# Optimization experiments

Hardware: AMD Instinct MI355X
Metric: run time of the kernel (lower is better)

The kernel has to match this reference:

```python
import jax, jax.numpy as jnp
import numpy as np
from jax import lax

UNITS = 64
LAYERS = 4

def _lstm_layer(x, Wx, U, b):
    # x: [B,T,F]; Keras gate order i,f,c,o; activation=relu, recurrent_activation=sigmoid
    B = x.shape[0]
    xz = jnp.einsum('btf,fg->btg', x, Wx) + b  # precompute input projections [B,T,4U]
    def step(carry, xz_t):
        h, c = carry
        z = xz_t + h @ U
        i, f, g, o = jnp.split(z, 4, axis=-1)
        c = jax.nn.sigmoid(f) * c + jax.nn.sigmoid(i) * jax.nn.relu(g)
        h = jax.nn.sigmoid(o) * jax.nn.relu(c)
        return (h, c), h
    h0 = jnp.zeros((B, UNITS), dtype=x.dtype)
    c0 = jnp.zeros((B, UNITS), dtype=x.dtype)
    _, hs = lax.scan(step, (h0, c0), jnp.swapaxes(xz, 0, 1))
    return jnp.swapaxes(hs, 0, 1)  # [B,T,U]

def setup_inputs() -> dict:
    key = jax.random.key(0)
    ks = jax.random.split(key, 1 + 3 * LAYERS + 2)
    B, T, F = 1024, 512, 1
    d = {'x': jax.random.normal(ks[0], (B, T, F), dtype=jnp.float32)}
    fin = F
    for l in range(LAYERS):
        d[f'Wx{l}'] = jax.random.normal(ks[1 + 3 * l], (fin, 4 * UNITS), dtype=jnp.float32) * 0.05
        d[f'U{l}'] = jax.random.normal(ks[2 + 3 * l], (UNITS, 4 * UNITS), dtype=jnp.float32) * 0.05
        d[f'b{l}'] = jnp.zeros((4 * UNITS,), dtype=jnp.float32)
        fin = UNITS
    d['Wd'] = jax.random.normal(ks[-2], (UNITS, 1), dtype=jnp.float32) * 0.05
    d['bd'] = jnp.zeros((1,), dtype=jnp.float32)
    return d

def reference(x, Wx0, U0, b0, Wx1, U1, b1, Wx2, U2, b2, Wx3, U3, b3, Wd, bd):
    # Dropout is identity at inference.
    h = x
    for Wx, U, b in ((Wx0, U0, b0), (Wx1, U1, b1), (Wx2, U2, b2), (Wx3, U3, b3)):
        h = _lstm_layer(h, Wx, U, b)
    h_last = h[:, -1, :]  # return_sequences=False on last LSTM
    return h_last @ Wd + bd  # [B,1]
```

## Files before the change

kernel.cpp:

```cpp
#include <hip/hip_runtime.h>
#include <stdint.h>

#define TT 512

typedef __fp16   f16x8  __attribute__((ext_vector_type(8)));
typedef float    f32x4  __attribute__((ext_vector_type(4)));
typedef __fp16   fp16x2 __attribute__((ext_vector_type(2)));
typedef uint32_t u32x2  __attribute__((ext_vector_type(2)));

__device__ __forceinline__ f32x4 mfma16(f16x8 a, f16x8 b, f32x4 c) {
    return __builtin_amdgcn_mfma_f32_16x16x32_f16(a, b, c, 0, 0, 0);
}
__device__ __forceinline__ uint32_t pkf16(float a, float b) {
    fp16x2 h = __builtin_amdgcn_cvt_pkrtz(a, b);
    return __builtin_bit_cast(uint32_t, h);
}

#define REP8(M) M(0)M(1)M(2)M(3)M(4)M(5)M(6)M(7)

#define GA(SRC, T, F, SC) (f16x8){ \
  (__fp16)((SRC)[(32*(F)+8*quad+0)*256 + 16*(T)+l15] * (SC)), \
  (__fp16)((SRC)[(32*(F)+8*quad+1)*256 + 16*(T)+l15] * (SC)), \
  (__fp16)((SRC)[(32*(F)+8*quad+2)*256 + 16*(T)+l15] * (SC)), \
  (__fp16)((SRC)[(32*(F)+8*quad+3)*256 + 16*(T)+l15] * (SC)), \
  (__fp16)((SRC)[(32*(F)+8*quad+4)*256 + 16*(T)+l15] * (SC)), \
  (__fp16)((SRC)[(32*(F)+8*quad+5)*256 + 16*(T)+l15] * (SC)), \
  (__fp16)((SRC)[(32*(F)+8*quad+6)*256 + 16*(T)+l15] * (SC)), \
  (__fp16)((SRC)[(32*(F)+8*quad+7)*256 + 16*(T)+l15] * (SC)) }

#define DECLT(j) f16x8 uA##j##_0, uA##j##_1, wA##j##_0, wA##j##_1; f32x4 bias##j;
#define LOADT(j) { \
  const int Tg_ = ((j)>>1)*4 + 2*h + ((j)&1); \
  const float sc_ = (((j)>>1) == 2) ? 1.0f : -1.4426950408889634f; \
  uA##j##_0 = GA(Uw, Tg_, 0, sc_); uA##j##_1 = GA(Uw, Tg_, 1, sc_); \
  bias##j = (f32x4){ bw_[16*Tg_ + 4*quad + 0] * sc_, bw_[16*Tg_ + 4*quad + 1] * sc_, \
                     bw_[16*Tg_ + 4*quad + 2] * sc_, bw_[16*Tg_ + 4*quad + 3] * sc_ }; \
  if (l > 0) { wA##j##_0 = GA(Wsrc, Tg_, 0, sc_); wA##j##_1 = GA(Wsrc, Tg_, 1, sc_); } \
  else { wA##j##_0 = __builtin_bit_cast(f16x8, (f32x4){ \
           Wx0[16*Tg_+4*quad+0] * sc_, Wx0[16*Tg_+4*quad+1] * sc_, \
           Wx0[16*Tg_+4*quad+2] * sc_, Wx0[16*Tg_+4*quad+3] * sc_ }); \
         wA##j##_1 = wA##j##_0; } }

#define MW0(j) acc##j = mfma16(wA##j##_0, xBp0, bias##j);
#define MW1(j) acc##j = mfma16(wA##j##_1, xBp1, acc##j);
#define MX(j)  acc##j = bias##j + __builtin_bit_cast(f32x4, wA##j##_0) * xvp4;
#define MU0(j) acc##j = mfma16(uA##j##_0, hB0, acc##j);
#define MU1(j) acc##j = mfma16(uA##j##_1, hB1, acc##j);

#define MFMA_SEG(t_) { \
  const __fp16* hp_ = hb_l + (((t_)-1)&7)*1152 + l15*72 + 8*quad; \
  f16x8 hB0 = *(const f16x8*)hp_; \
  f16x8 hB1 = *(const f16x8*)(hp_ + 32); \
  if (l > 0) { REP8(MW0) REP8(MW1) } \
  else       { f32x4 xvp4 = {xvp, xvp, xvp, xvp}; REP8(MX) } \
  REP8(MU0) \
  REP8(MU1) }

#define GATES(qp, Ai, Af, Ag, Ao, CST, SAVEK, HK) { \
  f32x4 ei_, ef_, eo_; \
  _Pragma("unroll") for (int r_ = 0; r_ < 4; ++r_) { \
    ei_[r_] = __builtin_amdgcn_exp2f(Ai[r_]); \
    ef_[r_] = __builtin_amdgcn_exp2f(Af[r_]); \
    eo_[r_] = __builtin_amdgcn_exp2f(Ao[r_]); \
  } \
  f32x4 si_, sf_, so_; \
  _Pragma("unroll") for (int r_ = 0; r_ < 4; ++r_) { \
    si_[r_] = __builtin_amdgcn_rcpf(1.0f + ei_[r_]); \
    sf_[r_] = __builtin_amdgcn_rcpf(1.0f + ef_[r_]); \
    so_[r_] = __builtin_amdgcn_rcpf(1.0f + eo_[r_]); \
  } \
  const f32x4 z4_ = {0.f, 0.f, 0.f, 0.f}; \
  f32x4 rg_ = __builtin_elementwise_max(Ag, z4_); \
  f32x4 cv_ = sf_ * CST + si_ * rg_; \
  CST = cv_; \
  f32x4 hv_ = so_ * __builtin_elementwise_max(cv_, z4_); \
  u32x2 pv_ = { pkf16(hv_[0], hv_[1]), pkf16(hv_[2], hv_[3]) }; \
  *(u32x2*)(hw_ + 16*(qp)) = pv_; \
  if (SAVEK) HK = hv_; }

#define GATE_SEG(tg_, SV_) { \
  __fp16* hw_ = hb_l + ((tg_)&7)*1152 + l15*72 + 32*h + 4*quad; \
  GATES(0, acc0, acc2, acc4, acc6, cst0, SV_, hK0) \
  GATES(1, acc1, acc3, acc5, acc7, cst1, SV_, hK1) }

#define WAITGE(cache, idx, need) \
  while ((cache) < (need)) \
    (cache) = __hip_atomic_load(&Pf[idx], __ATOMIC_ACQUIRE, __HIP_MEMORY_SCOPE_WORKGROUP);

__global__ __launch_bounds__(512)
__attribute__((amdgpu_waves_per_eu(2, 2)))
void lstm_phase(
    const float* __restrict__ x,
    const float* __restrict__ Wx0, const float* __restrict__ U0, const float* __restrict__ b0,
    const float* __restrict__ Wx1, const float* __restrict__ U1, const float* __restrict__ b1,
    const float* __restrict__ Wx2, const float* __restrict__ U2, const float* __restrict__ b2,
    const float* __restrict__ Wx3, const float* __restrict__ U3, const float* __restrict__ b3,
    const float* __restrict__ Wd,  const float* __restrict__ bd,
    float* __restrict__ out)
{
    extern __shared__ uint32_t smem[];
    __fp16* hb16 = (__fp16*)smem;
    float*  xs   = (float*)(smem + 18432);
    float*  red  = (float*)(smem + 27136);
    int*    Pf   = (int*)(smem + 27168);

    const int tid  = threadIdx.x;
    const int lane = tid & 63;
    const int l15  = lane & 15;
    const int quad = lane >> 4;
    const int wv   = tid >> 6;
    const int l    = wv >> 1;
    const int h    = wv & 1;
    const int b0i  = blockIdx.x * 16;

    for (int i = tid; i < 27176; i += 512) smem[i] = 0;
    __syncthreads();
    for (int i = tid; i < 16 * TT; i += 512) {
        int row = i >> 9, t_ = i & (TT - 1);
        xs[t_ * 17 + row] = x[(b0i + row) * TT + t_];
    }

    const float* Uw   = (l == 0) ? U0 : (l == 1) ? U1 : (l == 2) ? U2 : U3;
    const float* bw_  = (l == 0) ? b0 : (l == 1) ? b1 : (l == 2) ? b2 : b3;
    const float* Wsrc = (l == 1) ? Wx1 : (l == 2) ? Wx2 : (l == 3) ? Wx3 : U0;

    REP8(DECLT)
    REP8(LOADT)

    f32x4 acc0, acc1, acc2, acc3, acc4, acc5, acc6, acc7;
    f32x4 cst0 = {0,0,0,0}, cst1 = {0,0,0,0};
    f32x4 hK0  = {0,0,0,0}, hK1  = {0,0,0,0};

    __fp16* hb_l  = hb16 + l * 9216;
    const __fp16* hb_in = hb16 + (l > 0 ? (l - 1) * 9216 : 0);

    f16x8 xBp0 = {}, xBp1 = {};
    float xvp = 0.f;

    __syncthreads();

    if (l == 0) xvp = xs[l15];

    int pA0 = 0, pA1 = 0, pP = 0, pC0 = 0, pC1 = 0;

    for (int t = 0; t < TT; ++t) {
        if (l > 0) {
            WAITGE(pA0, 2*l - 2, t + 1)
            WAITGE(pA1, 2*l - 1, t + 1)
            const __fp16* xp_ = hb_in + (t & 7) * 1152 + l15 * 72 + 8 * quad;
            xBp0 = *(const f16x8*)xp_;
            xBp1 = *(const f16x8*)(xp_ + 32);
        }
        if (t > 0) WAITGE(pP, 2*l + 1 - h, t)
        if (l < 3 && t >= 8) {
            WAITGE(pC0, 2*l + 2, t - 7)
            WAITGE(pC1, 2*l + 3, t - 7)
        }
        __builtin_amdgcn_s_setprio(1);
        MFMA_SEG(t)
        __builtin_amdgcn_s_setprio(0);
        {
            const bool sv_ = (l == 3) && (t == TT - 1);
            GATE_SEG(t, sv_)
        }
        __hip_atomic_store(&Pf[2*l + h], t + 1, __ATOMIC_RELEASE, __HIP_MEMORY_SCOPE_WORKGROUP);
        if (l == 0 && t + 1 < TT) xvp = xs[(t + 1) * 17 + l15];
    }

    __syncthreads();

    if (l == 3) {
        float p = 0.f;
        #pragma unroll
        for (int r = 0; r < 4; ++r) {
            p += hK0[r] * Wd[32 * h + 4 * quad + r];
            p += hK1[r] * Wd[32 * h + 16 + 4 * quad + r];
        }
        p += __shfl_down(p, 32, 64);
        p += __shfl_down(p, 16, 64);
        if (lane < 16) red[h * 16 + lane] = p;
    }
    __syncthreads();
    if (wv == 6 && lane < 16) out[b0i + lane] = red[lane] + red[16 + lane] + bd[0];
}

extern "C" void kernel_launch(void* const* d_in, const int* in_sizes, int n_in,
                              void* d_out, int out_size, void* d_ws, size_t ws_size,
                              hipStream_t stream) {
    const float* x   = (const float*)d_in[0];
    const float* Wx0 = (const float*)d_in[1];
    const float* U0  = (const float*)d_in[2];
    const float* b0  = (const float*)d_in[3];
    const float* Wx1 = (const float*)d_in[4];
    const float* U1  = (const float*)d_in[5];
    const float* b1  = (const float*)d_in[6];
    const float* Wx2 = (const float*)d_in[7];
    const float* U2  = (const float*)d_in[8];
    const float* b2  = (const float*)d_in[9];
    const float* Wx3 = (const float*)d_in[10];
    const float* U3  = (const float*)d_in[11];
    const float* b3  = (const float*)d_in[12];
    const float* Wd  = (const float*)d_in[13];
    const float* bd  = (const float*)d_in[14];
    float* out = (float*)d_out;

    static const int kLds = 27176 * 4;
    (void)hipFuncSetAttribute((const void*)lstm_phase,
                              hipFuncAttributeMaxDynamicSharedMemorySize, kLds);
    hipLaunchKernelGGL(lstm_phase, dim3(64), dim3(512), kLds, stream,
                       x, Wx0, U0, b0, Wx1, U1, b1, Wx2, U2, b2, Wx3, U3, b3,
                       Wd, bd, out);
}
```

Baseline: 638.5 us.

## Split each LSTM layer across four waves instead of two per workgroup

Doubles the block to 1024 threads so each layer's gate computation is spread over four waves, each owning a 16-unit slice, with half as many MFMAs and gate evaluations per wave per timestep. Biases move from registers to LDS and are reloaded every step to free registers for the higher wave count. Per-wave progress flags replace per-pair flags, so each wave now polls three sibling flags plus four upstream and four downstream flags. The aim is to shorten the serial per-step critical path, at the cost of more synchronisation polling and LDS traffic.

New measurement: 1.095 ms. +71.4%, slower.

```diff
diff --git a/kernel.cpp b/kernel.cpp
--- a/kernel.cpp
+++ b/kernel.cpp
@@ -16,7 +16,7 @@
     return __builtin_bit_cast(uint32_t, h);
 }
 
-#define REP8(M) M(0)M(1)M(2)M(3)M(4)M(5)M(6)M(7)
+#define REP4(M) M(0)M(1)M(2)M(3)
 
 #define GA(SRC, T, F, SC) (f16x8){ \
   (__fp16)((SRC)[(32*(F)+8*quad+0)*256 + 16*(T)+l15] * (SC)), \
@@ -28,13 +28,11 @@
   (__fp16)((SRC)[(32*(F)+8*quad+6)*256 + 16*(T)+l15] * (SC)), \
   (__fp16)((SRC)[(32*(F)+8*quad+7)*256 + 16*(T)+l15] * (SC)) }
 
-#define DECLT(j) f16x8 uA##j##_0, uA##j##_1, wA##j##_0, wA##j##_1; f32x4 bias##j;
+#define DECLT(j) f16x8 uA##j##_0, uA##j##_1, wA##j##_0, wA##j##_1;
 #define LOADT(j) { \
-  const int Tg_ = ((j)>>1)*4 + 2*h + ((j)&1); \
-  const float sc_ = (((j)>>1) == 2) ? 1.0f : -1.4426950408889634f; \
+  const int Tg_ = 4*(j) + w; \
+  const float sc_ = ((j) == 2) ? 1.0f : -1.4426950408889634f; \
   uA##j##_0 = GA(Uw, Tg_, 0, sc_); uA##j##_1 = GA(Uw, Tg_, 1, sc_); \
-  bias##j = (f32x4){ bw_[16*Tg_ + 4*quad + 0] * sc_, bw_[16*Tg_ + 4*quad + 1] * sc_, \
-                     bw_[16*Tg_ + 4*quad + 2] * sc_, bw_[16*Tg_ + 4*quad + 3] * sc_ }; \
   if (l > 0) { wA##j##_0 = GA(Wsrc, Tg_, 0, sc_); wA##j##_1 = GA(Wsrc, Tg_, 1, sc_); } \
   else { wA##j##_0 = __builtin_bit_cast(f16x8, (f32x4){ \
            Wx0[16*Tg_+4*quad+0] * sc_, Wx0[16*Tg_+4*quad+1] * sc_, \
@@ -48,20 +46,24 @@
 #define MU1(j) acc##j = mfma16(uA##j##_1, hB1, acc##j);
 
 #define MFMA_SEG(t_) { \
+  f32x4 bias0 = *(const f32x4*)(bsl +   0); \
+  f32x4 bias1 = *(const f32x4*)(bsl +  64); \
+  f32x4 bias2 = *(const f32x4*)(bsl + 128); \
+  f32x4 bias3 = *(const f32x4*)(bsl + 192); \
   const __fp16* hp_ = hb_l + (((t_)-1)&7)*1152 + l15*72 + 8*quad; \
   f16x8 hB0 = *(const f16x8*)hp_; \
   f16x8 hB1 = *(const f16x8*)(hp_ + 32); \
-  if (l > 0) { REP8(MW0) REP8(MW1) } \
-  else       { f32x4 xvp4 = {xvp, xvp, xvp, xvp}; REP8(MX) } \
-  REP8(MU0) \
-  REP8(MU1) }
-
-#define GATES(qp, Ai, Af, Ag, Ao, CST, SAVEK, HK) { \
+  if (l > 0) { REP4(MW0) REP4(MW1) } \
+  else       { f32x4 xvp4 = {xvp, xvp, xvp, xvp}; REP4(MX) } \
+  REP4(MU0) \
+  REP4(MU1) }
+
+#define GATE_SEG(tg_, SV_) { \
   f32x4 ei_, ef_, eo_; \
   _Pragma("unroll") for (int r_ = 0; r_ < 4; ++r_) { \
-    ei_[r_] = __builtin_amdgcn_exp2f(Ai[r_]); \
-    ef_[r_] = __builtin_amdgcn_exp2f(Af[r_]); \
-    eo_[r_] = __builtin_amdgcn_exp2f(Ao[r_]); \
+    ei_[r_] = __builtin_amdgcn_exp2f(acc0[r_]); \
+    ef_[r_] = __builtin_amdgcn_exp2f(acc1[r_]); \
+    eo_[r_] = __builtin_amdgcn_exp2f(acc3[r_]); \
   } \
   f32x4 si_, sf_, so_; \
   _Pragma("unroll") for (int r_ = 0; r_ < 4; ++r_) { \
@@ -70,25 +72,19 @@
     so_[r_] = __builtin_amdgcn_rcpf(1.0f + eo_[r_]); \
   } \
   const f32x4 z4_ = {0.f, 0.f, 0.f, 0.f}; \
-  f32x4 rg_ = __builtin_elementwise_max(Ag, z4_); \
-  f32x4 cv_ = sf_ * CST + si_ * rg_; \
-  CST = cv_; \
+  f32x4 rg_ = __builtin_elementwise_max(acc2, z4_); \
+  f32x4 cv_ = sf_ * cst0 + si_ * rg_; \
+  cst0 = cv_; \
   f32x4 hv_ = so_ * __builtin_elementwise_max(cv_, z4_); \
   u32x2 pv_ = { pkf16(hv_[0], hv_[1]), pkf16(hv_[2], hv_[3]) }; \
-  *(u32x2*)(hw_ + 16*(qp)) = pv_; \
-  if (SAVEK) HK = hv_; }
-
-#define GATE_SEG(tg_, SV_) { \
-  __fp16* hw_ = hb_l + ((tg_)&7)*1152 + l15*72 + 32*h + 4*quad; \
-  GATES(0, acc0, acc2, acc4, acc6, cst0, SV_, hK0) \
-  GATES(1, acc1, acc3, acc5, acc7, cst1, SV_, hK1) }
-
-#define WAITGE(cache, idx, need) \
-  while ((cache) < (need)) \
-    (cache) = __hip_atomic_load(&Pf[idx], __ATOMIC_ACQUIRE, __HIP_MEMORY_SCOPE_WORKGROUP);
-
-__global__ __launch_bounds__(512)
-__attribute__((amdgpu_waves_per_eu(2, 2)))
+  __fp16* hw_ = hb_l + ((tg_)&7)*1152 + l15*72 + 16*w + 4*quad; \
+  *(u32x2*)hw_ = pv_; \
+  if (SV_) hK0 = hv_; }
+
+#define PLOAD(idx) __hip_atomic_load(&Pw[idx], __ATOMIC_ACQUIRE, __HIP_MEMORY_SCOPE_WORKGROUP)
+
+__global__ __launch_bounds__(1024)
+__attribute__((amdgpu_waves_per_eu(4, 4)))
 void lstm_phase(
     const float* __restrict__ x,
     const float* __restrict__ Wx0, const float* __restrict__ U0, const float* __restrict__ b0,
@@ -102,37 +98,44 @@
     __fp16* hb16 = (__fp16*)smem;
     float*  xs   = (float*)(smem + 18432);
     float*  red  = (float*)(smem + 27136);
-    int*    Pf   = (int*)(smem + 27168);
+    float*  bs   = (float*)(smem + 27200);
+    int*    Pw   = (int*)(smem + 28224);
 
     const int tid  = threadIdx.x;
     const int lane = tid & 63;
     const int l15  = lane & 15;
     const int quad = lane >> 4;
     const int wv   = tid >> 6;
-    const int l    = wv >> 1;
-    const int h    = wv & 1;
+    const int l    = wv >> 2;
+    const int w    = wv & 3;
     const int b0i  = blockIdx.x * 16;
 
-    for (int i = tid; i < 27176; i += 512) smem[i] = 0;
-    __syncthreads();
-    for (int i = tid; i < 16 * TT; i += 512) {
+    for (int i = tid; i < 28240; i += 1024) smem[i] = 0;
+    __syncthreads();
+    for (int i = tid; i < 16 * TT; i += 1024) {
         int row = i >> 9, t_ = i & (TT - 1);
         xs[t_ * 17 + row] = x[(b0i + row) * TT + t_];
     }
+    {
+        int l_ = tid >> 8, c_ = tid & 255;
+        const float* bsrc = (l_ == 0) ? b0 : (l_ == 1) ? b1 : (l_ == 2) ? b2 : b3;
+        float sc_ = ((c_ >> 6) == 2) ? 1.0f : -1.4426950408889634f;
+        bs[tid] = bsrc[c_] * sc_;
+    }
 
     const float* Uw   = (l == 0) ? U0 : (l == 1) ? U1 : (l == 2) ? U2 : U3;
-    const float* bw_  = (l == 0) ? b0 : (l == 1) ? b1 : (l == 2) ? b2 : b3;
     const float* Wsrc = (l == 1) ? Wx1 : (l == 2) ? Wx2 : (l == 3) ? Wx3 : U0;
 
-    REP8(DECLT)
-    REP8(LOADT)
-
-    f32x4 acc0, acc1, acc2, acc3, acc4, acc5, acc6, acc7;
-    f32x4 cst0 = {0,0,0,0}, cst1 = {0,0,0,0};
-    f32x4 hK0  = {0,0,0,0}, hK1  = {0,0,0,0};
+    REP4(DECLT)
+    REP4(LOADT)
+
+    f32x4 acc0, acc1, acc2, acc3;
+    f32x4 cst0 = {0,0,0,0};
+    f32x4 hK0  = {0,0,0,0};
 
     __fp16* hb_l  = hb16 + l * 9216;
     const __fp16* hb_in = hb16 + (l > 0 ? (l - 1) * 9216 : 0);
+    const float*  bsl   = bs + l * 256 + 16 * w + 4 * quad;
 
     f16x8 xBp0 = {}, xBp1 = {};
     float xvp = 0.f;
@@ -141,20 +144,36 @@
 
     if (l == 0) xvp = xs[l15];
 
-    int pA0 = 0, pA1 = 0, pP = 0, pC0 = 0, pC1 = 0;
+    int pS0 = 0, pS1 = 0, pS2 = 0;
+    int pI0 = 0, pI1 = 0, pI2 = 0, pI3 = 0;
+    int pO0 = 0, pO1 = 0, pO2 = 0, pO3 = 0;
+    const int k0 = 4*l + ((w + 1) & 3), k1 = 4*l + ((w + 2) & 3), k2 = 4*l + ((w + 3) & 3);
 
     for (int t = 0; t < TT; ++t) {
         if (l > 0) {
-            WAITGE(pA0, 2*l - 2, t + 1)
-            WAITGE(pA1, 2*l - 1, t + 1)
+            if (pI0 <= t || pI1 <= t || pI2 <= t || pI3 <= t) {
+                do {
+                    pI0 = PLOAD(4*l - 4); pI1 = PLOAD(4*l - 3);
+                    pI2 = PLOAD(4*l - 2); pI3 = PLOAD(4*l - 1);
+                } while (pI0 <= t || pI1 <= t || pI2 <= t || pI3 <= t);
+            }
             const __fp16* xp_ = hb_in + (t & 7) * 1152 + l15 * 72 + 8 * quad;
             xBp0 = *(const f16x8*)xp_;
             xBp1 = *(const f16x8*)(xp_ + 32);
         }
-        if (t > 0) WAITGE(pP, 2*l + 1 - h, t)
+        if (t > 0 && (pS0 < t || pS1 < t || pS2 < t)) {
+            do {
+                pS0 = PLOAD(k0); pS1 = PLOAD(k1); pS2 = PLOAD(k2);
+            } while (pS0 < t || pS1 < t || pS2 < t);
+        }
         if (l < 3 && t >= 8) {
-            WAITGE(pC0, 2*l + 2, t - 7)
-            WAITGE(pC1, 2*l + 3, t - 7)
+            const int need = t - 7;
+            if (pO0 < need || pO1 < need || pO2 < need || pO3 < need) {
+                do {
+                    pO0 = PLOAD(4*l + 4); pO1 = PLOAD(4*l + 5);
+                    pO2 = PLOAD(4*l + 6); pO3 = PLOAD(4*l + 7);
+                } while (pO0 < need || pO1 < need || pO2 < need || pO3 < need);
+            }
         }
         __builtin_amdgcn_s_setprio(1);
         MFMA_SEG(t)
@@ -163,25 +182,35 @@
             const bool sv_ = (l == 3) && (t == TT - 1);
             GATE_SEG(t, sv_)
         }
-        __hip_atomic_store(&Pf[2*l + h], t + 1, __ATOMIC_RELEASE, __HIP_MEMORY_SCOPE_WORKGROUP);
+        __hip_atomic_store(&Pw[wv], t + 1, __ATOMIC_RELEASE, __HIP_MEMORY_SCOPE_WORKGROUP);
         if (l == 0 && t + 1 < TT) xvp = xs[(t + 1) * 17 + l15];
     }
 
     __syncthreads();
 
     if (l == 3) {
+        float* hsv = (float*)(smem + 18432);
+        *(f32x4*)(hsv + (w * 64 + lane) * 4) = hK0;
+    }
+    __syncthreads();
+    if (l == 3 && w < 2) {
+        const int h = w;
+        const float* hsv = (const float*)(smem + 18432);
+        f32x4 hk0 = *(const f32x4*)(hsv + ((2 * h)     * 64 + lane) * 4);
+        f32x4 hk1 = *(const f32x4*)(hsv + ((2 * h + 1) * 64 + lane) * 4);
         float p = 0.f;
         #pragma unroll
         for (int r = 0; r < 4; ++r) {
-            p += hK0[r] * Wd[32 * h + 4 * quad + r];
-            p += hK1[r] * Wd[32 * h + 16 + 4 * quad + r];
+            p += hk0[r] * Wd[32 * h + 4 * quad + r];
+            p += hk1[r] * Wd[32 * h + 16 + 4 * quad + r];
         }
         p += __shfl_down(p, 32, 64);
         p += __shfl_down(p, 16, 64);
         if (lane < 16) red[h * 16 + lane] = p;
     }
     __syncthreads();
-    if (wv == 6 && lane < 16) out[b0i + lane] = red[lane] + red[16 + lane] + bd[0];
+    if (wv == 0 && lane < 16)
+        out[b0i + lane] = red[lane] + red[16 + lane] + bd[0];
 }
 
 extern "C" void kernel_launch(void* const* d_in, const int* in_sizes, int n_in,
@@ -204,10 +233,10 @@
     const float* bd  = (const float*)d_in[14];
     float* out = (float*)d_out;
 
-    static const int kLds = 27176 * 4;
+    static const int kLds = 28240 * 4;
     (void)hipFuncSetAttribute((const void*)lstm_phase,
                               hipFuncAttributeMaxDynamicSharedMemorySize, kLds);
-    hipLaunchKernelGGL(lstm_phase, dim3(64), dim3(512), kLds, stream,
+    hipLaunchKernelGGL(lstm_phase, dim3(64), dim3(1024), kLds, stream,
                        x, Wx0, U0, b0, Wx1, U1, b1, Wx2, U2, b2, Wx3, U3, b3,
                        Wd, bd, out);
 }
```
